# Kernel tuning notes

Measured on AMD Instinct MI355X. Metric: run time of the kernel, lower is better.

Reference implementation:

```python
import jax, jax.numpy as jnp
import numpy as np

B, S, E = 16384, 32, 128
H, DH, O = 4, 32, 128  # num_heads, head_dim (qkv_features//num_heads), out_features


def setup_inputs() -> dict:
    key = jax.random.key(0)
    kx, kq, kk, kv, ko = jax.random.split(key, 5)
    return {
        "x": jax.random.normal(kx, (B, S, E), dtype=jnp.float32),
        "w_q": jax.random.normal(kq, (H, E, DH), dtype=jnp.float32),
        "w_k": jax.random.normal(kk, (H, E, DH), dtype=jnp.float32),
        "w_v": jax.random.normal(kv, (H, E, DH), dtype=jnp.float32),
        "w_o": jax.random.normal(ko, (H, DH, O), dtype=jnp.float32),
    }


def reference(x, w_q, w_k, w_v, w_o):
    # Per-head projections: [B, H, S, DH]
    scale = jnp.asarray(w_q.shape[-1] ** -0.5, x.dtype)
    Q = jnp.einsum("bse,hed->bhsd", x, w_q) * scale
    K = jnp.einsum("bse,hed->bhsd", x, w_k)
    V = jnp.einsum("bse,hed->bhsd", x, w_v)
    scores = jnp.einsum("bhsd,bhtd->bhst", Q, K)  # [B, H, S, S]
    A = jax.nn.softmax(scores, axis=-1)
    Hd = jnp.einsum("bhst,bhtd->bhsd", A, V)  # [B, H, S, DH]
    # Per-head output projection, summed across heads: [B, S, O]
    out = jnp.einsum("bhsd,hdo->bso", Hd, w_o)
    return out
```

## Files before the change

### kernel.cpp

```cpp
#include <hip/hip_runtime.h>


typedef __bf16 bf16x8 __attribute__((ext_vector_type(8)));
typedef __bf16 bf16x2 __attribute__((ext_vector_type(2)));
typedef float f32x4 __attribute__((ext_vector_type(4)));

union FragU { unsigned int w[4]; bf16x8 v; };

__device__ inline unsigned short f2bf(float f) {
  return __builtin_bit_cast(unsigned short, (__bf16)f);
}
__device__ inline float bf2f(unsigned short h) {
  return __builtin_bit_cast(float, (unsigned int)h << 16);
}

__device__ inline bf16x8 ld_frag8(const unsigned short* p) {
  FragU f;
  const uint2* q = (const uint2*)p;
  uint2 a = q[0], b = q[1];
  f.w[0] = a.x; f.w[1] = a.y; f.w[2] = b.x; f.w[3] = b.y;
  return f.v;
}
__device__ inline bf16x8 ld_frag16(const unsigned short* p) {
  FragU f;
  uint4 a = *(const uint4*)p;
  f.w[0] = a.x; f.w[1] = a.y; f.w[2] = a.z; f.w[3] = a.w;
  return f.v;
}

__device__ inline f32x4 mfma16(bf16x8 a, bf16x8 b, f32x4 c) {
  return __builtin_amdgcn_mfma_f32_16x16x32_bf16(a, b, c, 0, 0, 0);
}

__device__ inline void wb_pair(unsigned short* dhi, unsigned short* dlo, float v) {
  __bf16 h = (__bf16)v;
  *dhi = __builtin_bit_cast(unsigned short, h);
  *dlo = f2bf(v - (float)h);
}

#define SYNC_LDS() do { asm volatile("s_waitcnt lgkmcnt(0)" ::: "memory"); \
                        __builtin_amdgcn_s_barrier(); \
                        asm volatile("" ::: "memory"); } while (0)
#define SYNC_VM()  do { asm volatile("s_waitcnt vmcnt(0) lgkmcnt(0)" ::: "memory"); \
                        __builtin_amdgcn_s_barrier(); \
                        asm volatile("" ::: "memory"); } while (0)

__device__ inline void stage4(const unsigned short* wt, unsigned short* ldsb,
                              int widu, int lane) {
  const char* g = (const char*)wt + (widu << 12) + (lane << 4);
  char* l = (char*)ldsb + (widu << 12);
#pragma unroll
  for (int j = 0; j < 4; ++j) {
    __builtin_amdgcn_global_load_lds(
        (const __attribute__((address_space(1))) void*)(g + (j << 10)),
        (__attribute__((address_space(3))) void*)(l + (j << 10)),
        16, 0, 0);
  }
}

__device__ inline void proj3(const unsigned short* lds, int col, int quad,
                             const bf16x8* xh, const bf16x8* xl,
                             f32x4& c0, f32x4& c1) {
#pragma unroll
  for (int kk = 0; kk < 4; ++kk) {
    int swz = ((((kk << 2) | quad) ^ col) << 3);
    const unsigned short* ph = lds + (col << 7) + swz;
    bf16x8 f0 = ld_frag16(ph);
    bf16x8 f1 = ld_frag16(ph + 2048);
    bf16x8 g0 = ld_frag16(ph + 4096);
    bf16x8 g1 = ld_frag16(ph + 6144);
    c0 = mfma16(xh[kk], f0, c0); c0 = mfma16(xl[kk], f0, c0); c0 = mfma16(xh[kk], g0, c0);
    c1 = mfma16(xh[kk], f1, c1); c1 = mfma16(xl[kk], f1, c1); c1 = mfma16(xh[kk], g1, c1);
  }
}

__global__ void prep_w(const float* __restrict__ wq, const float* __restrict__ wk,
                       const float* __restrict__ wv, const float* __restrict__ wo,
                       unsigned short* __restrict__ wsb) {
  int idx = blockIdx.x * 256 + threadIdx.x;
  int t = idx >> 14;
  int rem = idx & 16383;
  int hh = rem >> 12;
  int r2 = rem & 4095;
  const float* src = (t == 0) ? wq : (t == 1) ? wk : (t == 2) ? wv : wo;
  float v = src[rem];
  if (t == 0) v *= 0.17677669529663687f;
  int phys;
  if (t < 3) {
    int e = r2 >> 5, d = r2 & 31;
    phys = (d << 7) + (((e >> 3) ^ (d & 15)) << 3) + (e & 7);
  } else {
    int dh = r2 >> 7, o = r2 & 127;
    phys = (o << 5) + (((dh >> 3) ^ ((o >> 1) & 3)) << 3) + (dh & 7);
  }
  int base = ((t << 2) | hh) << 13;
  __bf16 h = (__bf16)v;
  wsb[base + phys] = __builtin_bit_cast(unsigned short, h);
  wsb[base + 4096 + phys] = f2bf(v - (float)h);
}

#define OFF_WB_HI 0
#define OFF_WB_LO 4096
#define OFF_A     8192
#define OFF_K_HI  10496
#define OFF_K_LO  12800
#define OFF_VT_HI 15104
#define OFF_VT_LO 17408
#define OFF_Q_HI  19712
#define OFF_Q_LO  22016
#define LDS_TOT   24320

__global__ __launch_bounds__(256, 3) void attn_fused(
    const float* __restrict__ x, const unsigned short* __restrict__ wsb,
    float* __restrict__ out) {
  __shared__ __align__(16) unsigned short lds[LDS_TOT];
  const int tid = threadIdx.x;
  const int lane = tid & 63;
  const int wid = tid >> 6;
  const int widu = __builtin_amdgcn_readfirstlane(wid);
  const int bl = wid >> 1;
  const int hw = wid & 1;
  const int sbase = hw << 4;
  const int col = lane & 15;
  const int quad = lane >> 4;

  bf16x8 xh[4], xl[4];
  for (int b = 0; b < 2; ++b) {
    const float4* xg = (const float4*)(x + ((long)(blockIdx.x * 2 + b) << 12));
#pragma unroll
    for (int it = 0; it < 4; ++it) {
      int f4 = it * 256 + tid;
      float4 v = xg[f4];
      int s = f4 >> 5;
      int e = (f4 & 31) << 2;
      __bf16 h0 = (__bf16)v.x, h1 = (__bf16)v.y, h2 = (__bf16)v.z, h3 = (__bf16)v.w;
      bf16x2 hp0 = {h0, h1}, hp1 = {h2, h3};
      bf16x2 lp0 = {(__bf16)(v.x - (float)h0), (__bf16)(v.y - (float)h1)};
      bf16x2 lp1 = {(__bf16)(v.z - (float)h2), (__bf16)(v.w - (float)h3)};
      uint2 ph = {__builtin_bit_cast(unsigned int, hp0), __builtin_bit_cast(unsigned int, hp1)};
      uint2 pl = {__builtin_bit_cast(unsigned int, lp0), __builtin_bit_cast(unsigned int, lp1)};
      *(uint2*)(lds + s * 132 + e) = ph;
      *(uint2*)(lds + 4224 + s * 132 + e) = pl;
    }
    __syncthreads();
    if (bl == b) {
#pragma unroll
      for (int kk = 0; kk < 4; ++kk) {
        xh[kk] = ld_frag8(lds + (sbase + col) * 132 + (kk << 5) + (quad << 3));
        xl[kk] = ld_frag8(lds + 4224 + (sbase + col) * 132 + (kk << 5) + (quad << 3));
      }
    }
    __syncthreads();
  }

  const long batch = (long)blockIdx.x * 2 + bl;
  const f32x4 zero = {0.f, 0.f, 0.f, 0.f};
  f32x4 oacc[8];
#pragma unroll
  for (int i = 0; i < 8; ++i) oacc[i] = zero;

  unsigned short* Kh = lds + OFF_K_HI + bl * 1152;
  unsigned short* Kl = lds + OFF_K_LO + bl * 1152;
  unsigned short* Vh = lds + OFF_VT_HI + bl * 1152;
  unsigned short* Vl = lds + OFF_VT_LO + bl * 1152;
  unsigned short* Qh = lds + OFF_Q_HI + (bl * 2 + hw) * 576;
  unsigned short* Ql = lds + OFF_Q_LO + (bl * 2 + hw) * 576;
  unsigned short* Abuf = lds + OFF_A + bl * 1152;

  for (int hh = 0; hh < 4; ++hh) {
    SYNC_LDS();
    stage4(wsb + (hh << 13), lds, widu, lane);
    SYNC_VM();

    f32x4 c0 = zero, c1 = zero;
    __builtin_amdgcn_s_setprio(1);
    proj3(lds, col, quad, xh, xl, c0, c1);
    __builtin_amdgcn_s_setprio(0);

    SYNC_LDS();
    stage4(wsb + ((4 + hh) << 13), lds, widu, lane);
#pragma unroll
    for (int r = 0; r < 4; ++r) {
      int row = (quad << 2) + r;
      wb_pair(Qh + row * 36 + col, Ql + row * 36 + col, c0[r]);
      wb_pair(Qh + row * 36 + col + 16, Ql + row * 36 + col + 16, c1[r]);
    }
    SYNC_VM();

    c0 = zero; c1 = zero;
    __builtin_amdgcn_s_setprio(1);
    proj3(lds, col, quad, xh, xl, c0, c1);
    __builtin_amdgcn_s_setprio(0);

    SYNC_LDS();
    stage4(wsb + ((8 + hh) << 13), lds, widu, lane);
#pragma unroll
    for (int r = 0; r < 4; ++r) {
      int row = sbase + (quad << 2) + r;
      wb_pair(Kh + row * 36 + col, Kl + row * 36 + col, c0[r]);
      wb_pair(Kh + row * 36 + col + 16, Kl + row * 36 + col + 16, c1[r]);
    }
    SYNC_VM();

    c0 = zero; c1 = zero;
    __builtin_amdgcn_s_setprio(1);
    proj3(lds, col, quad, xh, xl, c0, c1);
    __builtin_amdgcn_s_setprio(0);

    SYNC_LDS();
    stage4(wsb + ((12 + hh) << 13), lds, widu, lane);
#pragma unroll
    for (int r = 0; r < 4; ++r) {
      int t = sbase + (quad << 2) + r;
      wb_pair(Vh + col * 36 + t, Vl + col * 36 + t, c0[r]);
      wb_pair(Vh + (col + 16) * 36 + t, Vl + (col + 16) * 36 + t, c1[r]);
    }

    f32x4 s0 = zero, s1 = zero;
    {
      bf16x8 qhf = ld_frag8(Qh + col * 36 + (quad << 3));
      bf16x8 qlf = ld_frag8(Ql + col * 36 + (quad << 3));
      bf16x8 k0 = ld_frag8(Kh + col * 36 + (quad << 3));
      bf16x8 k1 = ld_frag8(Kh + (col + 16) * 36 + (quad << 3));
      bf16x8 k0l = ld_frag8(Kl + col * 36 + (quad << 3));
      bf16x8 k1l = ld_frag8(Kl + (col + 16) * 36 + (quad << 3));
      s0 = mfma16(qhf, k0, s0); s0 = mfma16(qlf, k0, s0); s0 = mfma16(qhf, k0l, s0);
      s1 = mfma16(qhf, k1, s1); s1 = mfma16(qlf, k1, s1); s1 = mfma16(qhf, k1l, s1);
    }
    float a0[4], a1[4];
#pragma unroll
    for (int r = 0; r < 4; ++r) {
      float v0 = s0[r], v1 = s1[r];
      float mx = fmaxf(v0, v1);
#pragma unroll
      for (int dx = 1; dx < 16; dx <<= 1) mx = fmaxf(mx, __shfl_xor(mx, dx));
      float e0 = __expf(v0 - mx), e1 = __expf(v1 - mx);
      float sm = e0 + e1;
#pragma unroll
      for (int dx = 1; dx < 16; dx <<= 1) sm += __shfl_xor(sm, dx);
      float inv = 1.0f / sm;
      a0[r] = e0 * inv; a1[r] = e1 * inv;
    }
#pragma unroll
    for (int r = 0; r < 4; ++r) {
      int row = sbase + (quad << 2) + r;
      Abuf[row * 36 + col] = f2bf(a0[r]);
      Abuf[row * 36 + col + 16] = f2bf(a1[r]);
    }
    SYNC_VM();

    f32x4 hv0 = zero, hv1 = zero;
    {
      bf16x8 af = ld_frag8(Abuf + (sbase + col) * 36 + (quad << 3));
      bf16x8 v0h = ld_frag8(Vh + col * 36 + (quad << 3));
      bf16x8 v1h = ld_frag8(Vh + (col + 16) * 36 + (quad << 3));
      bf16x8 v0l = ld_frag8(Vl + col * 36 + (quad << 3));
      bf16x8 v1l = ld_frag8(Vl + (col + 16) * 36 + (quad << 3));
      hv0 = mfma16(af, v0h, hv0); hv0 = mfma16(af, v0l, hv0);
      hv1 = mfma16(af, v1h, hv1); hv1 = mfma16(af, v1l, hv1);
    }
#pragma unroll
    for (int r = 0; r < 4; ++r) {
      int row = (quad << 2) + r;
      wb_pair(Qh + row * 36 + col, Ql + row * 36 + col, hv0[r]);
      wb_pair(Qh + row * 36 + col + 16, Ql + row * 36 + col + 16, hv1[r]);
    }
    {
      bf16x8 dh = ld_frag8(Qh + col * 36 + (quad << 3));
      bf16x8 dl = ld_frag8(Ql + col * 36 + (quad << 3));
      int swzo = (quad ^ ((col >> 1) & 3)) << 3;
      __builtin_amdgcn_s_setprio(1);
#pragma unroll
      for (int t8 = 0; t8 < 8; ++t8) {
        const unsigned short* wp = lds + (((t8 << 4) + col) << 5) + swzo;
        bf16x8 wh = ld_frag16(wp);
        bf16x8 wl = ld_frag16(wp + 4096);
        oacc[t8] = mfma16(dh, wh, oacc[t8]);
        oacc[t8] = mfma16(dl, wh, oacc[t8]);
        oacc[t8] = mfma16(dh, wl, oacc[t8]);
      }
      __builtin_amdgcn_s_setprio(0);
    }
  }

  float* og = out + batch * 4096;
#pragma unroll
  for (int t8 = 0; t8 < 8; ++t8) {
#pragma unroll
    for (int r = 0; r < 4; ++r) {
      og[(sbase + (quad << 2) + r) * 128 + (t8 << 4) + col] = oacc[t8][r];
    }
  }
}

extern "C" void kernel_launch(void* const* d_in, const int* in_sizes, int n_in,
                              void* d_out, int out_size, void* d_ws, size_t ws_size,
                              hipStream_t stream) {
  const float* x = (const float*)d_in[0];
  const float* wq = (const float*)d_in[1];
  const float* wk = (const float*)d_in[2];
  const float* wv = (const float*)d_in[3];
  const float* wo = (const float*)d_in[4];
  float* out = (float*)d_out;
  unsigned short* wsb = (unsigned short*)d_ws;
  hipLaunchKernelGGL(prep_w, dim3(256), dim3(256), 0, stream, wq, wk, wv, wo, wsb);
  hipLaunchKernelGGL(attn_fused, dim3(8192), dim3(256), 0, stream, x, wsb, out);
}
```

Measured before the change: 635.1 us.

## Split projections by head-dim column half and use DPP row reductions in softmax

Measured after the change: 598.1 us. -5.8%, faster.

```diff
diff --git a/kernel.cpp b/kernel.cpp
--- a/kernel.cpp
+++ b/kernel.cpp
@@ -38,6 +38,26 @@
   *dlo = f2bf(v - (float)h);
 }
 
+template <int CTRL>
+__device__ inline float dppf(float x) {
+  return __builtin_bit_cast(float,
+      __builtin_amdgcn_update_dpp(0, __builtin_bit_cast(int, x), CTRL, 0xF, 0xF, true));
+}
+__device__ inline float rowmax16(float v) {
+  v = fmaxf(v, dppf<0xB1>(v));
+  v = fmaxf(v, dppf<0x4E>(v));
+  v = fmaxf(v, dppf<0x124>(v));
+  v = fmaxf(v, dppf<0x128>(v));
+  return v;
+}
+__device__ inline float rowsum16(float v) {
+  v += dppf<0xB1>(v);
+  v += dppf<0x4E>(v);
+  v += dppf<0x124>(v);
+  v += dppf<0x128>(v);
+  return v;
+}
+
 #define SYNC_LDS() do { asm volatile("s_waitcnt lgkmcnt(0)" ::: "memory"); \
                         __builtin_amdgcn_s_barrier(); \
                         asm volatile("" ::: "memory"); } while (0)
@@ -58,19 +78,17 @@
   }
 }
 
-__device__ inline void proj3(const unsigned short* lds, int col, int quad,
-                             const bf16x8* xh, const bf16x8* xl,
-                             f32x4& c0, f32x4& c1) {
+__device__ inline void projNS(const unsigned short* wb, int col, int quad, int z,
+                              const bf16x8 xh[2][4], const bf16x8 xl[2][4],
+                              f32x4& c0, f32x4& c1) {
 #pragma unroll
   for (int kk = 0; kk < 4; ++kk) {
     int swz = ((((kk << 2) | quad) ^ col) << 3);
-    const unsigned short* ph = lds + (col << 7) + swz;
-    bf16x8 f0 = ld_frag16(ph);
-    bf16x8 f1 = ld_frag16(ph + 2048);
-    bf16x8 g0 = ld_frag16(ph + 4096);
-    bf16x8 g1 = ld_frag16(ph + 6144);
-    c0 = mfma16(xh[kk], f0, c0); c0 = mfma16(xl[kk], f0, c0); c0 = mfma16(xh[kk], g0, c0);
-    c1 = mfma16(xh[kk], f1, c1); c1 = mfma16(xl[kk], f1, c1); c1 = mfma16(xh[kk], g1, c1);
+    const unsigned short* ph = wb + (((z << 4) + col) << 7) + swz;
+    bf16x8 f = ld_frag16(ph);
+    bf16x8 g = ld_frag16(ph + 4096);
+    c0 = mfma16(xh[0][kk], f, c0); c0 = mfma16(xl[0][kk], f, c0); c0 = mfma16(xh[0][kk], g, c0);
+    c1 = mfma16(xh[1][kk], f, c1); c1 = mfma16(xl[1][kk], f, c1); c1 = mfma16(xh[1][kk], g, c1);
   }
 }
 
@@ -124,7 +142,7 @@
   const int col = lane & 15;
   const int quad = lane >> 4;
 
-  bf16x8 xh[4], xl[4];
+  bf16x8 xh[2][4], xl[2][4];
   for (int b = 0; b < 2; ++b) {
     const float4* xg = (const float4*)(x + ((long)(blockIdx.x * 2 + b) << 12));
 #pragma unroll
@@ -145,10 +163,12 @@
     __syncthreads();
     if (bl == b) {
 #pragma unroll
-      for (int kk = 0; kk < 4; ++kk) {
-        xh[kk] = ld_frag8(lds + (sbase + col) * 132 + (kk << 5) + (quad << 3));
-        xl[kk] = ld_frag8(lds + 4224 + (sbase + col) * 132 + (kk << 5) + (quad << 3));
-      }
+      for (int mt = 0; mt < 2; ++mt)
+#pragma unroll
+        for (int kk = 0; kk < 4; ++kk) {
+          xh[mt][kk] = ld_frag8(lds + ((mt << 4) + col) * 132 + (kk << 5) + (quad << 3));
+          xl[mt][kk] = ld_frag8(lds + 4224 + ((mt << 4) + col) * 132 + (kk << 5) + (quad << 3));
+        }
     }
     __syncthreads();
   }
@@ -163,8 +183,8 @@
   unsigned short* Kl = lds + OFF_K_LO + bl * 1152;
   unsigned short* Vh = lds + OFF_VT_HI + bl * 1152;
   unsigned short* Vl = lds + OFF_VT_LO + bl * 1152;
-  unsigned short* Qh = lds + OFF_Q_HI + (bl * 2 + hw) * 576;
-  unsigned short* Ql = lds + OFF_Q_LO + (bl * 2 + hw) * 576;
+  unsigned short* Qh = lds + OFF_Q_HI + bl * 1152;
+  unsigned short* Ql = lds + OFF_Q_LO + bl * 1152;
   unsigned short* Abuf = lds + OFF_A + bl * 1152;
 
   for (int hh = 0; hh < 4; ++hh) {
@@ -174,52 +194,65 @@
 
     f32x4 c0 = zero, c1 = zero;
     __builtin_amdgcn_s_setprio(1);
-    proj3(lds, col, quad, xh, xl, c0, c1);
+    projNS(lds, col, quad, hw, xh, xl, c0, c1);
     __builtin_amdgcn_s_setprio(0);
 
     SYNC_LDS();
     stage4(wsb + ((4 + hh) << 13), lds, widu, lane);
 #pragma unroll
-    for (int r = 0; r < 4; ++r) {
-      int row = (quad << 2) + r;
-      wb_pair(Qh + row * 36 + col, Ql + row * 36 + col, c0[r]);
-      wb_pair(Qh + row * 36 + col + 16, Ql + row * 36 + col + 16, c1[r]);
+    for (int mt = 0; mt < 2; ++mt) {
+      f32x4& c = mt ? c1 : c0;
+#pragma unroll
+      for (int r = 0; r < 4; ++r) {
+        int row = (mt << 4) + (quad << 2) + r;
+        wb_pair(Qh + row * 36 + sbase + col, Ql + row * 36 + sbase + col, c[r]);
+      }
     }
     SYNC_VM();
 
     c0 = zero; c1 = zero;
     __builtin_amdgcn_s_setprio(1);
-    proj3(lds, col, quad, xh, xl, c0, c1);
+    projNS(lds, col, quad, hw, xh, xl, c0, c1);
     __builtin_amdgcn_s_setprio(0);
 
     SYNC_LDS();
     stage4(wsb + ((8 + hh) << 13), lds, widu, lane);
 #pragma unroll
-    for (int r = 0; r < 4; ++r) {
-      int row = sbase + (quad << 2) + r;
-      wb_pair(Kh + row * 36 + col, Kl + row * 36 + col, c0[r]);
-      wb_pair(Kh + row * 36 + col + 16, Kl + row * 36 + col + 16, c1[r]);
+    for (int mt = 0; mt < 2; ++mt) {
+      f32x4& c = mt ? c1 : c0;
+#pragma unroll
+      for (int r = 0; r < 4; ++r) {
+        int row = (mt << 4) + (quad << 2) + r;
+        wb_pair(Kh + row * 36 + sbase + col, Kl + row * 36 + sbase + col, c[r]);
+      }
     }
     SYNC_VM();
 
     c0 = zero; c1 = zero;
     __builtin_amdgcn_s_setprio(1);
-    proj3(lds, col, quad, xh, xl, c0, c1);
+    projNS(lds, col, quad, hw, xh, xl, c0, c1);
     __builtin_amdgcn_s_setprio(0);
 
     SYNC_LDS();
     stage4(wsb + ((12 + hh) << 13), lds, widu, lane);
 #pragma unroll
-    for (int r = 0; r < 4; ++r) {
-      int t = sbase + (quad << 2) + r;
-      wb_pair(Vh + col * 36 + t, Vl + col * 36 + t, c0[r]);
-      wb_pair(Vh + (col + 16) * 36 + t, Vl + (col + 16) * 36 + t, c1[r]);
+    for (int mt = 0; mt < 2; ++mt) {
+      f32x4& c = mt ? c1 : c0;
+      __bf16 h0 = (__bf16)c[0], h1 = (__bf16)c[1], h2 = (__bf16)c[2], h3 = (__bf16)c[3];
+      bf16x2 hp0 = {h0, h1}, hp1 = {h2, h3};
+      bf16x2 lp0 = {(__bf16)(c[0] - (float)h0), (__bf16)(c[1] - (float)h1)};
+      bf16x2 lp1 = {(__bf16)(c[2] - (float)h2), (__bf16)(c[3] - (float)h3)};
+      int off = (sbase + col) * 36 + (mt << 4) + (quad << 2);
+      *(uint2*)(Vh + off) = make_uint2(__builtin_bit_cast(unsigned int, hp0),
+                                       __builtin_bit_cast(unsigned int, hp1));
+      *(uint2*)(Vl + off) = make_uint2(__builtin_bit_cast(unsigned int, lp0),
+                                       __builtin_bit_cast(unsigned int, lp1));
     }
 
     f32x4 s0 = zero, s1 = zero;
     {
-      bf16x8 qhf = ld_frag8(Qh + col * 36 + (quad << 3));
-      bf16x8 qlf = ld_frag8(Ql + col * 36 + (quad << 3));
+      bf16x8 qhf = ld_frag8(Qh + (sbase + col) * 36 + (quad << 3));
+      bf16x8 qlf = ld_frag8(Ql + (sbase + col) * 36 + (quad << 3));
       bf16x8 k0 = ld_frag8(Kh + col * 36 + (quad << 3));
       bf16x8 k1 = ld_frag8(Kh + (col + 16) * 36 + (quad << 3));
       bf16x8 k0l = ld_frag8(Kl + col * 36 + (quad << 3));
@@ -231,13 +264,9 @@
 #pragma unroll
     for (int r = 0; r < 4; ++r) {
       float v0 = s0[r], v1 = s1[r];
-      float mx = fmaxf(v0, v1);
-#pragma unroll
-      for (int dx = 1; dx < 16; dx <<= 1) mx = fmaxf(mx, __shfl_xor(mx, dx));
+      float mx = rowmax16(fmaxf(v0, v1));
       float e0 = __expf(v0 - mx), e1 = __expf(v1 - mx);
-      float sm = e0 + e1;
-#pragma unroll
-      for (int dx = 1; dx < 16; dx <<= 1) sm += __shfl_xor(sm, dx);
+      float sm = rowsum16(e0 + e1);
       float inv = 1.0f / sm;
       a0[r] = e0 * inv; a1[r] = e1 * inv;
     }
@@ -261,13 +290,13 @@
     }
 #pragma unroll
     for (int r = 0; r < 4; ++r) {
-      int row = (quad << 2) + r;
+      int row = sbase + (quad << 2) + r;
       wb_pair(Qh + row * 36 + col, Ql + row * 36 + col, hv0[r]);
       wb_pair(Qh + row * 36 + col + 16, Ql + row * 36 + col + 16, hv1[r]);
     }
     {
-      bf16x8 dh = ld_frag8(Qh + col * 36 + (quad << 3));
-      bf16x8 dl = ld_frag8(Ql + col * 36 + (quad << 3));
+      bf16x8 dh = ld_frag8(Qh + (sbase + col) * 36 + (quad << 3));
+      bf16x8 dl = ld_frag8(Ql + (sbase + col) * 36 + (quad << 3));
       int swzo = (quad ^ ((col >> 1) & 3)) << 3;
       __builtin_amdgcn_s_setprio(1);
 #pragma unroll
```
